# Performance work log

Hardware: AMD Instinct MI355X
Metric: run time of the kernel (lower is better)

Reference implementation:

```python
import jax, jax.numpy as jnp
import numpy as np

N, E, F_IN, H, C = 20000, 320000, 256, 4, 64
D = H * C  # hidden_dim = 256
NEG_SLOPE = 0.2
LN_EPS = 1e-5


def setup_inputs() -> dict:
    key = jax.random.key(0)
    ks = jax.random.split(key, 12)
    x = jax.random.normal(ks[0], (N, F_IN), dtype=jnp.float32)
    # edges guaranteed self-loop-free (PyG GATConv removes then re-adds self loops)
    dst = jax.random.randint(ks[1], (E,), 0, N)
    off = jax.random.randint(ks[2], (E,), 1, N)
    src = (dst + off) % N
    edge_index = jnp.stack([src, dst]).astype(jnp.int64)

    def lin(k, fan_in, shape):
        return jax.random.normal(k, shape, dtype=jnp.float32) / np.sqrt(fan_in)

    W1 = lin(ks[3], F_IN, (F_IN, D)); b1 = jnp.zeros((D,), jnp.float32)
    a_src1 = lin(ks[4], C, (H, C)); a_dst1 = lin(ks[5], C, (H, C))
    W2 = lin(ks[6], D, (D, D)); b2 = jnp.zeros((D,), jnp.float32)
    a_src2 = lin(ks[7], C, (H, C)); a_dst2 = lin(ks[8], C, (H, C))
    g1 = jnp.ones((D,), jnp.float32); be1 = jnp.zeros((D,), jnp.float32)
    g2 = jnp.ones((D,), jnp.float32); be2 = jnp.zeros((D,), jnp.float32)
    attn_w = lin(ks[9], D, (D, 1)); attn_b = jnp.zeros((1,), jnp.float32)
    return dict(x=x, edge_index=edge_index, W1=W1, b1=b1, a_src1=a_src1,
                a_dst1=a_dst1, W2=W2, b2=b2, a_src2=a_src2, a_dst2=a_dst2,
                g1=g1, be1=be1, g2=g2, be2=be2, attn_w=attn_w, attn_b=attn_b)


def _gat_conv(x, src, dst, W, b, a_src, a_dst):
    # x: [N, F] -> h: [N, H, C]
    h = (x @ W).reshape(N, H, C)
    alpha_s = jnp.einsum('nhc,hc->nh', h, a_src)  # [N, H]
    alpha_d = jnp.einsum('nhc,hc->nh', h, a_dst)
    e = jax.nn.leaky_relu(alpha_s[src] + alpha_d[dst], NEG_SLOPE)  # [E', H]
    # segment softmax over edges sharing a destination
    m = jax.ops.segment_max(e, dst, num_segments=N)
    w = jnp.exp(e - m[dst])
    z = jax.ops.segment_sum(w, dst, num_segments=N)
    alpha = w / (z[dst] + 1e-16)
    out = jax.ops.segment_sum(h[src] * alpha[:, :, None], dst, num_segments=N)
    return out.reshape(N, D) + b


def _layernorm(x, g, b):
    mu = x.mean(-1, keepdims=True)
    var = ((x - mu) ** 2).mean(-1, keepdims=True)
    return (x - mu) * jax.lax.rsqrt(var + LN_EPS) * g + b


def reference(x, edge_index, W1, b1, a_src1, a_dst1, W2, b2, a_src2, a_dst2,
              g1, be1, g2, be2, attn_w, attn_b):
    loops = jnp.arange(N, dtype=edge_index.dtype)
    src = jnp.concatenate([edge_index[0], loops])
    dst = jnp.concatenate([edge_index[1], loops])
    x1 = _gat_conv(x, src, dst, W1, b1, a_src1, a_dst1)
    x1 = jax.nn.elu(_layernorm(x1, g1, be1))
    x2 = _gat_conv(x1, src, dst, W2, b2, a_src2, a_dst2)
    x2 = jax.nn.elu(_layernorm(x2, g2, be2) + x1)
    attn = jax.nn.softmax(x2 @ attn_w + attn_b, axis=0)  # softmax over nodes
    pooled = (x2 * attn).sum(axis=0)  # [D]
    return pooled
```

## Files before the change

kernel.cpp:

```cpp
#include <hip/hip_runtime.h>
#include <math.h>

#define N_NODES 20000
#define E_EDGES 320000
#define TOT_E   (E_EDGES + N_NODES)
#define DHID    256
#define NHEAD   4
#define SCAN_NB ((N_NODES + 255) / 256)
#define SPART   32
#define ECAP    128

typedef float f32x4 __attribute__((ext_vector_type(4)));
typedef short short8 __attribute__((ext_vector_type(8)));
typedef unsigned short ushort;

__device__ __forceinline__ float wave_sum(float v) {
#pragma unroll
  for (int off = 32; off; off >>= 1) v += __shfl_xor(v, off);
  return v;
}
__device__ __forceinline__ ushort f2bf(float f) {
  unsigned u = __float_as_uint(f);
  u += 0x7fffu + ((u >> 16) & 1u);
  return (ushort)(u >> 16);
}
__device__ __forceinline__ float bflo(unsigned u) {
  return __uint_as_float(u << 16);
}
__device__ __forceinline__ float bfhi(unsigned u) {
  return __uint_as_float(u & 0xffff0000u);
}

__global__ void hist_kernel(const int* __restrict__ ei, int* __restrict__ deg) {
  int e = blockIdx.x * blockDim.x + threadIdx.x;
  if (e >= TOT_E) return;
  int dst = (e < E_EDGES) ? ei[E_EDGES + e] : (e - E_EDGES);
  atomicAdd(&deg[dst], 1);
}

__global__ __launch_bounds__(256)
void scan_blocks_kernel(const int* __restrict__ deg, int* __restrict__ bsum) {
  __shared__ int ws[4];
  const int t = threadIdx.x;
  const int i = blockIdx.x * 256 + t;
  int v = (i < N_NODES) ? deg[i] : 0;
  int s = v;
#pragma unroll
  for (int off = 32; off; off >>= 1) s += __shfl_xor(s, off);
  if ((t & 63) == 0) ws[t >> 6] = s;
  __syncthreads();
  if (t == 0) bsum[blockIdx.x] = ws[0] + ws[1] + ws[2] + ws[3];
}

__global__ __launch_bounds__(128)
void scan_tops_kernel(const int* __restrict__ bsum, int* __restrict__ boff) {
  __shared__ int tmp[SCAN_NB];
  const int t = threadIdx.x;
  if (t < SCAN_NB) tmp[t] = bsum[t];
  __syncthreads();
  if (t == 0) {
    int run = 0;
    for (int i = 0; i < SCAN_NB; ++i) { int x = tmp[i]; tmp[i] = run; run += x; }
  }
  __syncthreads();
  if (t < SCAN_NB) boff[t] = tmp[t];
}

__global__ __launch_bounds__(256)
void scan_apply_kernel(const int* __restrict__ deg, const int* __restrict__ boff,
                       int* __restrict__ rowp, int* __restrict__ cur) {
  __shared__ int ws[4];
  const int t = threadIdx.x;
  const int lane = t & 63, w = t >> 6;
  const int i = blockIdx.x * 256 + t;
  int v = (i < N_NODES) ? deg[i] : 0;
  int inc = v;
#pragma unroll
  for (int off = 1; off < 64; off <<= 1) {
    int u = __shfl_up(inc, off);
    if (lane >= off) inc += u;
  }
  if (lane == 63) ws[w] = inc;
  __syncthreads();
  int add = boff[blockIdx.x];
#pragma unroll
  for (int k = 0; k < 4; ++k)
    if (k < w) add += ws[k];
  int exc = add + inc - v;
  if (i < N_NODES) {
    rowp[i] = exc;
    cur[i] = exc;
    if (i == N_NODES - 1) rowp[N_NODES] = exc + v;
  }
}

__global__ void scatter_kernel(const int* __restrict__ ei, int* __restrict__ cur,
                               int* __restrict__ colb) {
  int e = blockIdx.x * blockDim.x + threadIdx.x;
  if (e >= TOT_E) return;
  int src, dst;
  if (e < E_EDGES) { src = ei[e]; dst = ei[E_EDGES + e]; }
  else             { src = dst = e - E_EDGES; }
  int pos = atomicAdd(&cur[dst], 1);
  colb[pos] = src;
}

__global__ __launch_bounds__(256)
void conv_inputs_kernel(const float* __restrict__ W1, const float* __restrict__ W2,
                        const float* __restrict__ x, ushort* __restrict__ Wt1,
                        ushort* __restrict__ Wt2, ushort* __restrict__ xb,
                        int* __restrict__ deg) {
  const int b = blockIdx.x;
  if (b < 512) {
    const float* W = (b < 256) ? W1 : W2;
    ushort* Wt = (b < 256) ? Wt1 : Wt2;
    const int n = b & 255;
    const int k = threadIdx.x;
    Wt[n * 256 + k] = f2bf(W[k * 256 + n]);
  } else if (b < 512 + N_NODES * 256 / 8 / 256) {
    int idx = (b - 512) * 256 + threadIdx.x;
    size_t base = (size_t)idx * 8;
    float4 a = *reinterpret_cast<const float4*>(x + base);
    float4 c = *reinterpret_cast<const float4*>(x + base + 4);
    short8 o;
    o[0] = f2bf(a.x); o[1] = f2bf(a.y); o[2] = f2bf(a.z); o[3] = f2bf(a.w);
    o[4] = f2bf(c.x); o[5] = f2bf(c.y); o[6] = f2bf(c.z); o[7] = f2bf(c.w);
    *reinterpret_cast<short8*>(xb + base) = o;
  } else {
    int idx = (b - (512 + N_NODES * 256 / 8 / 256)) * 256 + threadIdx.x;
    if (idx < N_NODES) deg[idx] = 0;
  }
}

__global__ __launch_bounds__(256)
void gemm_alpha_kernel(const ushort* __restrict__ Ab, const ushort* __restrict__ Wt,
                       const float* __restrict__ asrc, const float* __restrict__ adst,
                       ushort* __restrict__ hout, float* __restrict__ as_,
                       float* __restrict__ ad_) {
  __shared__ ushort hs[32 * 256];

  const int t = threadIdx.x;
  const int w = t >> 6;
  const int l = t & 63;
  const int row0 = blockIdx.x * 32;

  const ushort* abase = Ab + (size_t)(row0 + (l & 15)) * 256 + ((l >> 4) * 8);
  const ushort* bbase = Wt + (size_t)(w * 64 + (l & 15)) * 256 + ((l >> 4) * 8);

  f32x4 acc[2][4];
#pragma unroll
  for (int i = 0; i < 2; ++i)
#pragma unroll
    for (int j = 0; j < 4; ++j) acc[i][j] = (f32x4){0.f, 0.f, 0.f, 0.f};

  short8 a0 = *reinterpret_cast<const short8*>(abase);
  short8 a1 = *reinterpret_cast<const short8*>(abase + 16 * 256);
  short8 b0 = *reinterpret_cast<const short8*>(bbase);
  short8 b1 = *reinterpret_cast<const short8*>(bbase + 16 * 256);
  short8 b2 = *reinterpret_cast<const short8*>(bbase + 32 * 256);
  short8 b3 = *reinterpret_cast<const short8*>(bbase + 48 * 256);
#pragma unroll
  for (int kk = 0; kk < 256; kk += 32) {
    short8 na0, na1, nb0, nb1, nb2, nb3;
    if (kk + 32 < 256) {
      na0 = *reinterpret_cast<const short8*>(abase + kk + 32);
      na1 = *reinterpret_cast<const short8*>(abase + 16 * 256 + kk + 32);
      nb0 = *reinterpret_cast<const short8*>(bbase + kk + 32);
      nb1 = *reinterpret_cast<const short8*>(bbase + 16 * 256 + kk + 32);
      nb2 = *reinterpret_cast<const short8*>(bbase + 32 * 256 + kk + 32);
      nb3 = *reinterpret_cast<const short8*>(bbase + 48 * 256 + kk + 32);
    }
    acc[0][0] = __builtin_amdgcn_mfma_f32_16x16x32_bf16(a0, b0, acc[0][0], 0, 0, 0);
    acc[0][1] = __builtin_amdgcn_mfma_f32_16x16x32_bf16(a0, b1, acc[0][1], 0, 0, 0);
    acc[0][2] = __builtin_amdgcn_mfma_f32_16x16x32_bf16(a0, b2, acc[0][2], 0, 0, 0);
    acc[0][3] = __builtin_amdgcn_mfma_f32_16x16x32_bf16(a0, b3, acc[0][3], 0, 0, 0);
    acc[1][0] = __builtin_amdgcn_mfma_f32_16x16x32_bf16(a1, b0, acc[1][0], 0, 0, 0);
    acc[1][1] = __builtin_amdgcn_mfma_f32_16x16x32_bf16(a1, b1, acc[1][1], 0, 0, 0);
    acc[1][2] = __builtin_amdgcn_mfma_f32_16x16x32_bf16(a1, b2, acc[1][2], 0, 0, 0);
    acc[1][3] = __builtin_amdgcn_mfma_f32_16x16x32_bf16(a1, b3, acc[1][3], 0, 0, 0);
    if (kk + 32 < 256) {
      a0 = na0; a1 = na1; b0 = nb0; b1 = nb1; b2 = nb2; b3 = nb3;
    }
  }

  float asj[4], adj[4];
#pragma unroll
  for (int j = 0; j < 4; ++j) {
    asj[j] = asrc[w * 64 + j * 16 + (l & 15)];
    adj[j] = adst[w * 64 + j * 16 + (l & 15)];
  }
#pragma unroll
  for (int i = 0; i < 2; ++i) {
#pragma unroll
    for (int q = 0; q < 4; ++q) {
      float ps = 0.f, pd = 0.f;
#pragma unroll
      for (int j = 0; j < 4; ++j) {
        ps += acc[i][j][q] * asj[j];
        pd += acc[i][j][q] * adj[j];
      }
#pragma unroll
      for (int off = 1; off < 16; off <<= 1) {
        ps += __shfl_xor(ps, off);
        pd += __shfl_xor(pd, off);
      }
      int row = row0 + i * 16 + (l >> 4) * 4 + q;
      if ((l & 15) == 0) {
        as_[row * 4 + w] = ps;
        ad_[row * 4 + w] = pd;
      }
    }
  }

#pragma unroll
  for (int i = 0; i < 2; ++i)
#pragma unroll
    for (int j = 0; j < 4; ++j)
#pragma unroll
      for (int q = 0; q < 4; ++q) {
        int row = i * 16 + (l >> 4) * 4 + q;
        int col = w * 64 + j * 16 + (l & 15);
        hs[row * 256 + col] = f2bf(acc[i][j][q]);
      }
  __syncthreads();
#pragma unroll
  for (int g = 0; g < 4; ++g) {
    int gi = g * 256 + t;
    int row = gi >> 5;
    int slot = gi & 31;
    *reinterpret_cast<short8*>(hout + (size_t)(row0 + row) * 256 + slot * 8) =
        *reinterpret_cast<const short8*>(&hs[row * 256 + slot * 8]);
  }
}

__global__ __launch_bounds__(256)
void attn_gather_ln_kernel(const ushort* __restrict__ h, const float* __restrict__ as_,
                           const float* __restrict__ ad_, const int* __restrict__ rowp,
                           const int* __restrict__ colb, const float* __restrict__ bias,
                           const float* __restrict__ gamma, const float* __restrict__ beta,
                           const ushort* __restrict__ residb, ushort* __restrict__ outb,
                           const float* __restrict__ aw, const float* __restrict__ ab,
                           float* __restrict__ score) {
  __shared__ float ew[4][ECAP][NHEAD];
  __shared__ int   sidx[4][ECAP];

  const int t = threadIdx.x;
  const int wd = t >> 6;
  const int d = blockIdx.x * 4 + wd;
  const int l = t & 63;
  const int start = rowp[d];
  const int deg = rowp[d + 1] - start;
  const int* cb = colb + start;

  const int e16 = l >> 2, hh = l & 3;
  const float adv = ad_[d * 4 + hh];
  const int gh = l >> 4;
  const int c0 = l * 4;
  const ushort* hrow = h + c0;

  float zpart = 0.f;
  float a0 = 0.f, a1 = 0.f, a2 = 0.f, a3 = 0.f;

  for (int base = 0; base < deg; base += ECAP) {
    const int cnt = min(deg - base, ECAP);
    for (int i = e16; i < cnt; i += 16) {
      int s = cb[base + i];
      if (hh == 0) sidx[wd][i] = s;
      float e = as_[s * 4 + hh] + adv;
      e = (e >= 0.f) ? e : 0.2f * e;
      e = fminf(e, 60.f);
      float wv = __expf(e);
      ew[wd][i][hh] = wv;
      zpart += wv;
    }
    int i = 0;
    for (; i + 4 <= cnt; i += 4) {
      int s0 = sidx[wd][i], s1 = sidx[wd][i + 1];
      int s2 = sidx[wd][i + 2], s3 = sidx[wd][i + 3];
      float w0 = ew[wd][i][gh], w1 = ew[wd][i + 1][gh];
      float w2 = ew[wd][i + 2][gh], w3 = ew[wd][i + 3][gh];
      uint2 h0 = *reinterpret_cast<const uint2*>(hrow + (size_t)s0 * 256);
      uint2 h1 = *reinterpret_cast<const uint2*>(hrow + (size_t)s1 * 256);
      uint2 h2 = *reinterpret_cast<const uint2*>(hrow + (size_t)s2 * 256);
      uint2 h3 = *reinterpret_cast<const uint2*>(hrow + (size_t)s3 * 256);
      a0 += w0 * bflo(h0.x) + w1 * bflo(h1.x) + w2 * bflo(h2.x) + w3 * bflo(h3.x);
      a1 += w0 * bfhi(h0.x) + w1 * bfhi(h1.x) + w2 * bfhi(h2.x) + w3 * bfhi(h3.x);
      a2 += w0 * bflo(h0.y) + w1 * bflo(h1.y) + w2 * bflo(h2.y) + w3 * bflo(h3.y);
      a3 += w0 * bfhi(h0.y) + w1 * bfhi(h1.y) + w2 * bfhi(h2.y) + w3 * bfhi(h3.y);
    }
    for (; i < cnt; ++i) {
      int s = sidx[wd][i];
      float wv = ew[wd][i][gh];
      uint2 hv = *reinterpret_cast<const uint2*>(hrow + (size_t)s * 256);
      a0 += wv * bflo(hv.x);
      a1 += wv * bfhi(hv.x);
      a2 += wv * bflo(hv.y);
      a3 += wv * bfhi(hv.y);
    }
  }

#pragma unroll
  for (int off = 4; off < 64; off <<= 1) zpart += __shfl_xor(zpart, off);
  const float zi = 1.f / (__shfl(zpart, gh) + 1e-16f);

  float4 bi = *reinterpret_cast<const float4*>(bias + c0);
  float v0 = a0 * zi + bi.x, v1 = a1 * zi + bi.y;
  float v2 = a2 * zi + bi.z, v3 = a3 * zi + bi.w;

  float s1 = wave_sum(v0 + v1 + v2 + v3);
  float s2 = wave_sum(v0 * v0 + v1 * v1 + v2 * v2 + v3 * v3);
  float mu = s1 * (1.f / 256.f);
  float var = s2 * (1.f / 256.f) - mu * mu;
  float rstd = rsqrtf(var + 1e-5f);
  float4 ga = *reinterpret_cast<const float4*>(gamma + c0);
  float4 be = *reinterpret_cast<const float4*>(beta + c0);
  float y0 = (v0 - mu) * rstd * ga.x + be.x;
  float y1 = (v1 - mu) * rstd * ga.y + be.y;
  float y2 = (v2 - mu) * rstd * ga.z + be.z;
  float y3 = (v3 - mu) * rstd * ga.w + be.w;
  if (residb) {
    uint2 rv = *reinterpret_cast<const uint2*>(residb + (size_t)d * 256 + c0);
    y0 += bflo(rv.x); y1 += bfhi(rv.x); y2 += bflo(rv.y); y3 += bfhi(rv.y);
  }
  y0 = (y0 > 0.f) ? y0 : expm1f(y0);
  y1 = (y1 > 0.f) ? y1 : expm1f(y1);
  y2 = (y2 > 0.f) ? y2 : expm1f(y2);
  y3 = (y3 > 0.f) ? y3 : expm1f(y3);

  uint2 o;
  o.x = ((unsigned)f2bf(y0)) | (((unsigned)f2bf(y1)) << 16);
  o.y = ((unsigned)f2bf(y2)) | (((unsigned)f2bf(y3)) << 16);
  *reinterpret_cast<uint2*>(outb + (size_t)d * 256 + c0) = o;

  if (score) {
    float4 aww = *reinterpret_cast<const float4*>(aw + c0);
    float sp = wave_sum(y0 * aww.x + y1 * aww.y + y2 * aww.z + y3 * aww.w);
    if (l == 0) score[d] = sp + ab[0];
  }
}

__global__ __launch_bounds__(256)
void score_part_kernel(const float* __restrict__ s, float* __restrict__ pm,
                       float* __restrict__ pz) {
  __shared__ float red[4];
  const int t = threadIdx.x, b = blockIdx.x;
  const int lane = t & 63, wid = t >> 6;
  float m = -INFINITY;
  for (int n = b * 256 + t; n < N_NODES; n += SPART * 256) m = fmaxf(m, s[n]);
#pragma unroll
  for (int off = 32; off; off >>= 1) m = fmaxf(m, __shfl_xor(m, off));
  if (lane == 0) red[wid] = m;
  __syncthreads();
  m = fmaxf(fmaxf(red[0], red[1]), fmaxf(red[2], red[3]));
  __syncthreads();
  float z = 0.f;
  for (int n = b * 256 + t; n < N_NODES; n += SPART * 256) z += __expf(s[n] - m);
  z = wave_sum(z);
  if (lane == 0) red[wid] = z;
  __syncthreads();
  if (t == 0) { pm[b] = m; pz[b] = red[0] + red[1] + red[2] + red[3]; }
}

__global__ __launch_bounds__(64)
void score_comb_kernel(const float* __restrict__ pm, const float* __restrict__ pz,
                       float* __restrict__ mz) {
  const int l = threadIdx.x;
  float m = (l < SPART) ? pm[l] : -INFINITY;
#pragma unroll
  for (int off = 32; off; off >>= 1) m = fmaxf(m, __shfl_xor(m, off));
  float z = (l < SPART) ? pz[l] * __expf(pm[l] - m) : 0.f;
  z = wave_sum(z);
  if (l == 0) { mz[0] = m; mz[1] = z; }
}

__global__ __launch_bounds__(256)
void pool_partial_kernel(const ushort* __restrict__ hb2, const float* __restrict__ s,
                         const float* __restrict__ mz, float* __restrict__ part) {
  __shared__ float red4[4][256];
  const int t = threadIdx.x, b = blockIdx.x;
  const int c4 = t & 63, rsub = t >> 6;
  const float m = mz[0];
  const float invz = 1.f / mz[1];
  f32x4 acc = (f32x4){0.f, 0.f, 0.f, 0.f};
  for (int n = b * 4 + rsub; n < N_NODES; n += 1024) {
    float w = __expf(s[n] - m);
    uint2 hv = *reinterpret_cast<const uint2*>(hb2 + (size_t)n * 256 + c4 * 4);
    acc[0] += w * bflo(hv.x);
    acc[1] += w * bfhi(hv.x);
    acc[2] += w * bflo(hv.y);
    acc[3] += w * bfhi(hv.y);
  }
#pragma unroll
  for (int k = 0; k < 4; ++k) red4[rsub][c4 * 4 + k] = acc[k];
  __syncthreads();
  if (t < 256) {
    float v = red4[0][t] + red4[1][t] + red4[2][t] + red4[3][t];
    part[b * 256 + t] = v * invz;
  }
}

__global__ __launch_bounds__(256)
void pool_final_kernel(const float* __restrict__ part, float* __restrict__ out) {
  const int t = threadIdx.x;
  float acc = 0.f;
  for (int b = 0; b < 256; ++b) acc += part[b * 256 + t];
  out[t] = acc;
}

extern "C" void kernel_launch(void* const* d_in, const int* in_sizes, int n_in,
                              void* d_out, int out_size, void* d_ws, size_t ws_size,
                              hipStream_t stream) {
  const float* x      = (const float*)d_in[0];
  const int*   ei     = (const int*)d_in[1];
  const float* W1     = (const float*)d_in[2];
  const float* b1     = (const float*)d_in[3];
  const float* a_src1 = (const float*)d_in[4];
  const float* a_dst1 = (const float*)d_in[5];
  const float* W2     = (const float*)d_in[6];
  const float* b2     = (const float*)d_in[7];
  const float* a_src2 = (const float*)d_in[8];
  const float* a_dst2 = (const float*)d_in[9];
  const float* g1     = (const float*)d_in[10];
  const float* be1    = (const float*)d_in[11];
  const float* g2     = (const float*)d_in[12];
  const float* be2    = (const float*)d_in[13];
  const float* attn_w = (const float*)d_in[14];
  const float* attn_b = (const float*)d_in[15];
  float* out = (float*)d_out;

  char* p = (char*)d_ws;
  auto alloc = [&](size_t bytes) {
    char* r = p;
    p += (bytes + 255) & ~size_t(255);
    return r;
  };
  ushort* h   = (ushort*)alloc((size_t)N_NODES * 256 * 2);
  ushort* xb  = (ushort*)alloc((size_t)N_NODES * 256 * 2);
  ushort* xb1 = (ushort*)alloc((size_t)N_NODES * 256 * 2);
  ushort* hb2 = (ushort*)alloc((size_t)N_NODES * 256 * 2);
  float* as_  = (float*)alloc((size_t)N_NODES * 4 * 4);
  float* ad_  = (float*)alloc((size_t)N_NODES * 4 * 4);
  float* sbuf = (float*)alloc((size_t)N_NODES * 4);
  float* mz   = (float*)alloc(256);
  float* pm   = (float*)alloc((size_t)SPART * 4);
  float* pz   = (float*)alloc((size_t)SPART * 4);
  float* part = (float*)alloc((size_t)256 * 256 * 4);
  ushort* wt1 = (ushort*)alloc((size_t)256 * 256 * 2);
  ushort* wt2 = (ushort*)alloc((size_t)256 * 256 * 2);
  int* deg    = (int*)alloc((size_t)N_NODES * 4);
  int* rowp   = (int*)alloc((size_t)(N_NODES + 1) * 4);
  int* cur    = (int*)alloc((size_t)N_NODES * 4);
  int* colb   = (int*)alloc((size_t)TOT_E * 4);
  int* bsum   = (int*)alloc((size_t)SCAN_NB * 4);
  int* boff   = (int*)alloc((size_t)SCAN_NB * 4);

  const int EB = (TOT_E + 255) / 256;
  const int GB = N_NODES / 32;
  const int DB = N_NODES / 4;
  const int XB = N_NODES * 256 / 8 / 256;
  const int CONVB = 512 + XB + SCAN_NB;

  conv_inputs_kernel<<<CONVB, 256, 0, stream>>>(W1, W2, x, wt1, wt2, xb, deg);
  hist_kernel<<<EB, 256, 0, stream>>>(ei, deg);
  scan_blocks_kernel<<<SCAN_NB, 256, 0, stream>>>(deg, bsum);
  scan_tops_kernel<<<1, 128, 0, stream>>>(bsum, boff);
  scan_apply_kernel<<<SCAN_NB, 256, 0, stream>>>(deg, boff, rowp, cur);
  scatter_kernel<<<EB, 256, 0, stream>>>(ei, cur, colb);

  gemm_alpha_kernel<<<GB, 256, 0, stream>>>(xb, wt1, a_src1, a_dst1, h, as_, ad_);
  attn_gather_ln_kernel<<<DB, 256, 0, stream>>>(h, as_, ad_, rowp, colb, b1, g1, be1,
                                                nullptr, xb1, nullptr, nullptr, nullptr);
  gemm_alpha_kernel<<<GB, 256, 0, stream>>>(xb1, wt2, a_src2, a_dst2, h, as_, ad_);
  attn_gather_ln_kernel<<<DB, 256, 0, stream>>>(h, as_, ad_, rowp, colb, b2, g2, be2,
                                                xb1, hb2, attn_w, attn_b, sbuf);
  score_part_kernel<<<SPART, 256, 0, stream>>>(sbuf, pm, pz);
  score_comb_kernel<<<1, 64, 0, stream>>>(pm, pz, mz);
  pool_partial_kernel<<<256, 256, 0, stream>>>(hb2, sbuf, mz, part);
  pool_final_kernel<<<1, 256, 0, stream>>>(part, out);
}
```

Before: 173.6 us.

## Map each destination node to half a wave with 16-byte gathers and deeper unroll

The attention-gather-LayerNorm kernel now assigns 32 lanes per destination node instead of 64, so each lane handles 8 bf16 channels through 16-byte loads, and a block covers 8 nodes. The aggregation loop is unrolled by 8 to keep more independent gathers in flight, and the reductions use 32-lane shuffles. This targets the gather memory-latency bottleneck by using wider loads and more loads in flight per lane. The cost is more registers per thread and a smaller per-wave edge staging buffer (ECAP 64), which means more chunk iterations for high-degree nodes.

Measured after the change: 180.0 us. +3.7%, slower.

```diff
diff --git a/kernel.cpp b/kernel.cpp
--- a/kernel.cpp
+++ b/kernel.cpp
@@ -8,7 +8,7 @@
 #define NHEAD   4
 #define SCAN_NB ((N_NODES + 255) / 256)
 #define SPART   32
-#define ECAP    128
+#define ECAP    64
 
 typedef float f32x4 __attribute__((ext_vector_type(4)));
 typedef short short8 __attribute__((ext_vector_type(8)));
@@ -17,6 +17,11 @@
 __device__ __forceinline__ float wave_sum(float v) {
 #pragma unroll
   for (int off = 32; off; off >>= 1) v += __shfl_xor(v, off);
+  return v;
+}
+__device__ __forceinline__ float wave_sum32(float v) {
+#pragma unroll
+  for (int off = 16; off; off >>= 1) v += __shfl_xor(v, off);
   return v;
 }
 __device__ __forceinline__ ushort f2bf(float f) {
@@ -241,101 +246,127 @@
                            const ushort* __restrict__ residb, ushort* __restrict__ outb,
                            const float* __restrict__ aw, const float* __restrict__ ab,
                            float* __restrict__ score) {
-  __shared__ float ew[4][ECAP][NHEAD];
-  __shared__ int   sidx[4][ECAP];
+  __shared__ float ew[8][ECAP][NHEAD];
+  __shared__ int   sidx[8][ECAP];
 
   const int t = threadIdx.x;
-  const int wd = t >> 6;
-  const int d = blockIdx.x * 4 + wd;
+  const int ds = t >> 5;
+  const int d = blockIdx.x * 8 + ds;
+  const int q = t & 31;
   const int l = t & 63;
   const int start = rowp[d];
   const int deg = rowp[d + 1] - start;
   const int* cb = colb + start;
 
-  const int e16 = l >> 2, hh = l & 3;
+  const int e8 = q >> 2, hh = q & 3;
   const float adv = ad_[d * 4 + hh];
-  const int gh = l >> 4;
-  const int c0 = l * 4;
+  const int gh = q >> 3;
+  const int c0 = q * 8;
   const ushort* hrow = h + c0;
 
   float zpart = 0.f;
-  float a0 = 0.f, a1 = 0.f, a2 = 0.f, a3 = 0.f;
+  float a[8];
+#pragma unroll
+  for (int k = 0; k < 8; ++k) a[k] = 0.f;
 
   for (int base = 0; base < deg; base += ECAP) {
     const int cnt = min(deg - base, ECAP);
-    for (int i = e16; i < cnt; i += 16) {
+    for (int i = e8; i < cnt; i += 8) {
       int s = cb[base + i];
-      if (hh == 0) sidx[wd][i] = s;
+      if (hh == 0) sidx[ds][i] = s;
       float e = as_[s * 4 + hh] + adv;
       e = (e >= 0.f) ? e : 0.2f * e;
       e = fminf(e, 60.f);
       float wv = __expf(e);
-      ew[wd][i][hh] = wv;
+      ew[ds][i][hh] = wv;
       zpart += wv;
     }
     int i = 0;
+    for (; i + 8 <= cnt; i += 8) {
+      int ss[8]; float ww[8]; uint4 hv[8];
+#pragma unroll
+      for (int k = 0; k < 8; ++k) { ss[k] = sidx[ds][i + k]; ww[k] = ew[ds][i + k][gh]; }
+#pragma unroll
+      for (int k = 0; k < 8; ++k)
+        hv[k] = *reinterpret_cast<const uint4*>(hrow + (size_t)ss[k] * 256);
+#pragma unroll
+      for (int k = 0; k < 8; ++k) {
+        a[0] += ww[k] * bflo(hv[k].x); a[1] += ww[k] * bfhi(hv[k].x);
+        a[2] += ww[k] * bflo(hv[k].y); a[3] += ww[k] * bfhi(hv[k].y);
+        a[4] += ww[k] * bflo(hv[k].z); a[5] += ww[k] * bfhi(hv[k].z);
+        a[6] += ww[k] * bflo(hv[k].w); a[7] += ww[k] * bfhi(hv[k].w);
+      }
+    }
     for (; i + 4 <= cnt; i += 4) {
-      int s0 = sidx[wd][i], s1 = sidx[wd][i + 1];
-      int s2 = sidx[wd][i + 2], s3 = sidx[wd][i + 3];
-      float w0 = ew[wd][i][gh], w1 = ew[wd][i + 1][gh];
-      float w2 = ew[wd][i + 2][gh], w3 = ew[wd][i + 3][gh];
-      uint2 h0 = *reinterpret_cast<const uint2*>(hrow + (size_t)s0 * 256);
-      uint2 h1 = *reinterpret_cast<const uint2*>(hrow + (size_t)s1 * 256);
-      uint2 h2 = *reinterpret_cast<const uint2*>(hrow + (size_t)s2 * 256);
-      uint2 h3 = *reinterpret_cast<const uint2*>(hrow + (size_t)s3 * 256);
-      a0 += w0 * bflo(h0.x) + w1 * bflo(h1.x) + w2 * bflo(h2.x) + w3 * bflo(h3.x);
-      a1 += w0 * bfhi(h0.x) + w1 * bfhi(h1.x) + w2 * bfhi(h2.x) + w3 * bfhi(h3.x);
-      a2 += w0 * bflo(h0.y) + w1 * bflo(h1.y) + w2 * bflo(h2.y) + w3 * bflo(h3.y);
-      a3 += w0 * bfhi(h0.y) + w1 * bfhi(h1.y) + w2 * bfhi(h2.y) + w3 * bfhi(h3.y);
+      int ss[4]; float ww[4]; uint4 hv[4];
+#pragma unroll
+      for (int k = 0; k < 4; ++k) { ss[k] = sidx[ds][i + k]; ww[k] = ew[ds][i + k][gh]; }
+#pragma unroll
+      for (int k = 0; k < 4; ++k)
+        hv[k] = *reinterpret_cast<const uint4*>(hrow + (size_t)ss[k] * 256);
+#pragma unroll
+      for (int k = 0; k < 4; ++k) {
+        a[0] += ww[k] * bflo(hv[k].x); a[1] += ww[k] * bfhi(hv[k].x);
+        a[2] += ww[k] * bflo(hv[k].y); a[3] += ww[k] * bfhi(hv[k].y);
+        a[4] += ww[k] * bflo(hv[k].z); a[5] += ww[k] * bfhi(hv[k].z);
+        a[6] += ww[k] * bflo(hv[k].w); a[7] += ww[k] * bfhi(hv[k].w);
+      }
     }
     for (; i < cnt; ++i) {
-      int s = sidx[wd][i];
-      float wv = ew[wd][i][gh];
-      uint2 hv = *reinterpret_cast<const uint2*>(hrow + (size_t)s * 256);
-      a0 += wv * bflo(hv.x);
-      a1 += wv * bfhi(hv.x);
-      a2 += wv * bflo(hv.y);
-      a3 += wv * bfhi(hv.y);
-    }
-  }
-
-#pragma unroll
-  for (int off = 4; off < 64; off <<= 1) zpart += __shfl_xor(zpart, off);
-  const float zi = 1.f / (__shfl(zpart, gh) + 1e-16f);
-
-  float4 bi = *reinterpret_cast<const float4*>(bias + c0);
-  float v0 = a0 * zi + bi.x, v1 = a1 * zi + bi.y;
-  float v2 = a2 * zi + bi.z, v3 = a3 * zi + bi.w;
-
-  float s1 = wave_sum(v0 + v1 + v2 + v3);
-  float s2 = wave_sum(v0 * v0 + v1 * v1 + v2 * v2 + v3 * v3);
+      int s = sidx[ds][i];
+      float wv = ew[ds][i][gh];
+      uint4 hv = *reinterpret_cast<const uint4*>(hrow + (size_t)s * 256);
+      a[0] += wv * bflo(hv.x); a[1] += wv * bfhi(hv.x);
+      a[2] += wv * bflo(hv.y); a[3] += wv * bfhi(hv.y);
+      a[4] += wv * bflo(hv.z); a[5] += wv * bfhi(hv.z);
+      a[6] += wv * bflo(hv.w); a[7] += wv * bfhi(hv.w);
+    }
+  }
+
+#pragma unroll
+  for (int off = 4; off < 32; off <<= 1) zpart += __shfl_xor(zpart, off);
+  const float zi = 1.f / (__shfl(zpart, (l & 32) + gh) + 1e-16f);
+
+  float v[8];
+#pragma unroll
+  for (int k = 0; k < 8; ++k) v[k] = a[k] * zi + bias[c0 + k];
+
+  float ls = 0.f, lq = 0.f;
+#pragma unroll
+  for (int k = 0; k < 8; ++k) { ls += v[k]; lq += v[k] * v[k]; }
+  float s1 = wave_sum32(ls);
+  float s2 = wave_sum32(lq);
   float mu = s1 * (1.f / 256.f);
   float var = s2 * (1.f / 256.f) - mu * mu;
   float rstd = rsqrtf(var + 1e-5f);
-  float4 ga = *reinterpret_cast<const float4*>(gamma + c0);
-  float4 be = *reinterpret_cast<const float4*>(beta + c0);
-  float y0 = (v0 - mu) * rstd * ga.x + be.x;
-  float y1 = (v1 - mu) * rstd * ga.y + be.y;
-  float y2 = (v2 - mu) * rstd * ga.z + be.z;
-  float y3 = (v3 - mu) * rstd * ga.w + be.w;
+
+  float y[8];
+#pragma unroll
+  for (int k = 0; k < 8; ++k)
+    y[k] = (v[k] - mu) * rstd * gamma[c0 + k] + beta[c0 + k];
   if (residb) {
-    uint2 rv = *reinterpret_cast<const uint2*>(residb + (size_t)d * 256 + c0);
-    y0 += bflo(rv.x); y1 += bfhi(rv.x); y2 += bflo(rv.y); y3 += bfhi(rv.y);
-  }
-  y0 = (y0 > 0.f) ? y0 : expm1f(y0);
-  y1 = (y1 > 0.f) ? y1 : expm1f(y1);
-  y2 = (y2 > 0.f) ? y2 : expm1f(y2);
-  y3 = (y3 > 0.f) ? y3 : expm1f(y3);
-
-  uint2 o;
-  o.x = ((unsigned)f2bf(y0)) | (((unsigned)f2bf(y1)) << 16);
-  o.y = ((unsigned)f2bf(y2)) | (((unsigned)f2bf(y3)) << 16);
-  *reinterpret_cast<uint2*>(outb + (size_t)d * 256 + c0) = o;
+    uint4 rv = *reinterpret_cast<const uint4*>(residb + (size_t)d * 256 + c0);
+    y[0] += bflo(rv.x); y[1] += bfhi(rv.x);
+    y[2] += bflo(rv.y); y[3] += bfhi(rv.y);
+    y[4] += bflo(rv.z); y[5] += bfhi(rv.z);
+    y[6] += bflo(rv.w); y[7] += bfhi(rv.w);
+  }
+#pragma unroll
+  for (int k = 0; k < 8; ++k) y[k] = (y[k] > 0.f) ? y[k] : expm1f(y[k]);
+
+  uint4 o;
+  o.x = ((unsigned)f2bf(y[0])) | (((unsigned)f2bf(y[1])) << 16);
+  o.y = ((unsigned)f2bf(y[2])) | (((unsigned)f2bf(y[3])) << 16);
+  o.z = ((unsigned)f2bf(y[4])) | (((unsigned)f2bf(y[5])) << 16);
+  o.w = ((unsigned)f2bf(y[6])) | (((unsigned)f2bf(y[7])) << 16);
+  *reinterpret_cast<uint4*>(outb + (size_t)d * 256 + c0) = o;
 
   if (score) {
-    float4 aww = *reinterpret_cast<const float4*>(aw + c0);
-    float sp = wave_sum(y0 * aww.x + y1 * aww.y + y2 * aww.z + y3 * aww.w);
-    if (l == 0) score[d] = sp + ab[0];
+    float sp = 0.f;
+#pragma unroll
+    for (int k = 0; k < 8; ++k) sp += y[k] * aw[c0 + k];
+    sp = wave_sum32(sp);
+    if (q == 0) score[d] = sp + ab[0];
   }
 }
 
@@ -456,7 +487,7 @@
 
   const int EB = (TOT_E + 255) / 256;
   const int GB = N_NODES / 32;
-  const int DB = N_NODES / 4;
+  const int DB = N_NODES / 8;
   const int XB = N_NODES * 256 / 8 / 256;
   const int CONVB = 512 + XB + SCAN_NB;
 
```
